# Kernel tuning notes

Measured on AMD Instinct MI355X. Metric: run time of the kernel, lower is better.

## Reference

```python
import jax, jax.numpy as jnp
import numpy as np

N = 50000   # num nodes
E = 800000  # num edges (avg degree 16)
D = 128     # in = hidden = out channels


def setup_inputs() -> dict:
    key = jax.random.key(0)
    k0, k1, k2, k3, k4, k5 = jax.random.split(key, 6)
    x = jax.random.normal(k0, (N, D), dtype=jnp.float32)
    edge_index = jax.random.randint(k1, (2, E), 0, N, dtype=jnp.int32)
    scale = 1.0 / np.sqrt(D)
    W1 = jax.random.normal(k2, (D, D), dtype=jnp.float32) * scale
    b1 = jax.random.normal(k3, (D,), dtype=jnp.float32) * 0.01
    W2 = jax.random.normal(k4, (D, D), dtype=jnp.float32) * scale
    b2 = jax.random.normal(k5, (D,), dtype=jnp.float32) * 0.01
    return {"x": x, "edge_index": edge_index, "W1": W1, "b1": b1, "W2": W2, "b2": b2}


def reference(x, edge_index, W1, b1, W2, b2):
    n = x.shape[0]
    src, dst = edge_index[0], edge_index[1]
    # GCN adds self-loops before normalization
    loops = jnp.arange(n, dtype=src.dtype)
    s = jnp.concatenate([src, loops])
    d = jnp.concatenate([dst, loops])
    # symmetric normalization: deg^{-1/2}[s] * deg^{-1/2}[d]
    deg = jax.ops.segment_sum(jnp.ones_like(d, dtype=x.dtype), d, num_segments=n)
    dinv = jnp.where(deg > 0, jax.lax.rsqrt(deg), 0.0)
    ew = dinv[s] * dinv[d]  # [E+N]

    def gcn_conv(h, W, b):
        h = h @ W                                   # [N, D] dense transform first
        msg = ew[:, None] * h[s]                     # gather over edges [E+N, D]
        agg = jax.ops.segment_sum(msg, d, num_segments=n)  # scatter-add [N, D]
        return agg + b

    # layer 1: conv -> Identity BN -> ELU (dropout=0.0 -> no-op)
    h = jax.nn.elu(gcn_conv(x, W1, b1))
    # layer 2 (last): conv -> Identity BN -> ELU
    out = jax.nn.elu(gcn_conv(h, W2, b2))
    return out
```

## Files before the change

### kernel.cpp

```cpp
#include <hip/hip_runtime.h>
#include <math.h>

#define D 128
#define BCAP 8192
#define SLICE 64
#define PB 256

typedef __attribute__((ext_vector_type(8))) short bf16x8;
typedef __attribute__((ext_vector_type(4))) float f32x4;
typedef __attribute__((ext_vector_type(4))) unsigned int u32x4;


__device__ inline float2 bf2f2(unsigned int u) {
    union { unsigned int i; float f; } a, b;
    a.i = u << 16;
    b.i = u & 0xffff0000u;
    return make_float2(a.f, b.f);
}

__device__ inline unsigned short f2bf(float f) {
    union { float f; unsigned int i; } u;
    u.f = f;
    unsigned int r = u.i + 0x7fffu + ((u.i >> 16) & 1u);
    return (unsigned short)(r >> 16);
}

__device__ __forceinline__ float elu_fast(float r) {
    return r > 0.f ? r : __expf(r) - 1.f;
}


__device__ __forceinline__ void gemm_core(unsigned short (*Ws)[136], int gbid,
                                          const void* __restrict__ Ain, int a_fp32,
                                          unsigned int* __restrict__ Cb, int N) {
    const int tid = threadIdx.x;
    const int wid = tid >> 6;
    const int lane = tid & 63;
    const int quad = lane >> 4;
    const int ln = lane & 15;
    const int m = gbid * 64 + wid * 16 + ln;
    const bool valid = (m < N);

    f32x4 acc[8];
#pragma unroll
    for (int c = 0; c < 8; ++c) acc[c] = (f32x4){0.f, 0.f, 0.f, 0.f};

    __syncthreads();

#pragma unroll
    for (int ks = 0; ks < 4; ++ks) {
        const int k0 = ks * 32;
        bf16x8 af;
        if (a_fp32) {
            const float* A = (const float*)Ain;
            float4 lo = make_float4(0.f, 0.f, 0.f, 0.f), hi = lo;
            if (valid) {
                lo = *(const float4*)&A[(size_t)m * 128 + k0 + quad * 8];
                hi = *(const float4*)&A[(size_t)m * 128 + k0 + quad * 8 + 4];
            }
            af[0] = (short)f2bf(lo.x); af[1] = (short)f2bf(lo.y);
            af[2] = (short)f2bf(lo.z); af[3] = (short)f2bf(lo.w);
            af[4] = (short)f2bf(hi.x); af[5] = (short)f2bf(hi.y);
            af[6] = (short)f2bf(hi.z); af[7] = (short)f2bf(hi.w);
        } else {
            const uint4* A4 = (const uint4*)Ain;
            uint4 v = valid ? A4[(size_t)m * 16 + ks * 4 + quad]
                            : make_uint4(0u, 0u, 0u, 0u);
            union { uint4 u; bf16x8 h; } cv;
            cv.u = v;
            af = cv.h;
        }
#pragma unroll
        for (int c = 0; c < 8; ++c) {
            bf16x8 bf = *(const bf16x8*)&Ws[c * 16 + ln][k0 + quad * 8];
            acc[c] = __builtin_amdgcn_mfma_f32_16x16x32_bf16(af, bf, acc[c], 0, 0, 0);
        }
    }

    const int rowbase = gbid * 64 + wid * 16 + quad * 4;
#pragma unroll
    for (int c = 0; c < 8; ++c) {
#pragma unroll
        for (int r = 0; r < 4; ++r) {
            float v = acc[c][r];
            float vn = __shfl_xor(v, 1);
            int grow = rowbase + r;
            if (!(ln & 1) && grow < N) {
                unsigned int u = (unsigned int)f2bf(v) | ((unsigned int)f2bf(vn) << 16);
                Cb[(size_t)grow * 64 + c * 8 + (ln >> 1)] = u;
            }
        }
    }
}


__global__ __launch_bounds__(256) void k1_all(
        const int* __restrict__ src, const int* __restrict__ dst,
        const float* __restrict__ x, const float* __restrict__ W1,
        const float* __restrict__ W2, unsigned short* __restrict__ Wt2,
        unsigned int* __restrict__ pairs, unsigned char* __restrict__ cellCnt,
        unsigned int* __restrict__ hb1, int e, int chunk, int N, int gemmBlocks) {
    __shared__ __align__(16) unsigned char smem[128 * 136 * 2];
    const int tid = threadIdx.x;
    const int bid = blockIdx.x;

    if (bid < PB) {
        int* cur = (int*)smem;
        cur[tid] = 0;
        __syncthreads();
        const int e0 = bid * chunk;
        const int e1 = min(e0 + chunk, e);
        for (int i = e0 + tid; i < e1; i += 256) {
            int d = dst[i], s = src[i];
            int b = d >> 8;
            int off = atomicAdd(&cur[b], 1);
            if (off < SLICE)
                pairs[((size_t)(bid * 256 + b)) * SLICE + off] =
                    (unsigned int)s | ((unsigned int)(d & 255) << 16);
        }
        __syncthreads();
        cellCnt[bid * 256 + tid] = (unsigned char)min(cur[tid], SLICE);
    } else if (bid < PB + gemmBlocks) {
        unsigned short (*Ws)[136] = (unsigned short(*)[136])smem;
        for (int j = 0; j < 64; ++j) {
            int idx = tid + j * 256;
            Ws[idx & 127][idx >> 7] = f2bf(W1[idx]);
        }
        gemm_core(Ws, bid - PB, x, 1, hb1, N);
    } else {
        int i = (bid - PB - gemmBlocks) * 256 + tid;
        int k = i >> 7, n = i & 127;
        Wt2[n * 128 + k] = f2bf(W2[i]);
    }
}


__global__ __launch_bounds__(1024) void partB(const unsigned int* __restrict__ pairs,
                                              const unsigned char* __restrict__ cellCnt,
                                              unsigned short* __restrict__ col,
                                              unsigned int* __restrict__ meta,
                                              float* __restrict__ dinv, int n) {
    __shared__ unsigned int cellS[256][SLICE];
    __shared__ int cnt[256];
    __shared__ int deg[256];
    __shared__ int sc[256];
    __shared__ int cur[256];
    const int b = blockIdx.x;
    const int tid = threadIdx.x;
    const int cell0 = tid >> 6;
    const int slot = tid & 63;
    const int ch = tid >> 2;
    const int sub = tid & 3;

#pragma unroll
    for (int r = 0; r < 16; ++r) {
        const int cc = r * 16 + cell0;
        cellS[cc][slot] = pairs[((size_t)(cc * 256 + b)) * SLICE + slot];
    }
    if (tid < 256) {
        cnt[tid] = min((int)cellCnt[tid * 256 + b], SLICE);
        deg[tid] = 0;
    }
    __syncthreads();

    const int c = cnt[ch];
    for (int q = sub; q < c; q += 4) atomicAdd(&deg[cellS[ch][q] >> 16], 1);
    __syncthreads();

    if (tid < 256) sc[tid] = deg[tid];
    __syncthreads();
    for (int o = 1; o < 256; o <<= 1) {
        int t = 0;
        if (tid < 256 && tid >= o) t = sc[tid - o];
        __syncthreads();
        if (tid < 256) sc[tid] += t;
        __syncthreads();
    }
    if (tid < 256) {
        int v = deg[tid];
        int startw = sc[tid] - v;
        cur[tid] = startw;
        int node = b * 256 + tid;
        if (node < n) {
            meta[node] = ((unsigned int)(b * BCAP + startw) << 10) | (unsigned int)v;
            dinv[node] = rsqrtf((float)(v + 1));
        }
    }
    __syncthreads();

    for (int q = sub; q < c; q += 4) {
        unsigned int p = cellS[ch][q];
        int dl = p >> 16;
        int off = atomicAdd(&cur[dl], 1);
        col[(size_t)b * BCAP + off] = (unsigned short)(p & 0xffffu);
    }
}


__device__ __forceinline__ void fma8(float w, u32x4 u, f32x4& a, f32x4& b) {
    float2 v0 = bf2f2(u.x), v1 = bf2f2(u.y), v2 = bf2f2(u.z), v3 = bf2f2(u.w);
    a[0] = fmaf(w, v0.x, a[0]); a[1] = fmaf(w, v0.y, a[1]);
    a[2] = fmaf(w, v1.x, a[2]); a[3] = fmaf(w, v1.y, a[3]);
    b[0] = fmaf(w, v2.x, b[0]); b[1] = fmaf(w, v2.y, b[1]);
    b[2] = fmaf(w, v3.x, b[2]); b[3] = fmaf(w, v3.y, b[3]);
}

__device__ __forceinline__ void add8(u32x4 u, f32x4& a, f32x4& b) {
    float2 v0 = bf2f2(u.x), v1 = bf2f2(u.y), v2 = bf2f2(u.z), v3 = bf2f2(u.w);
    a[0] += v0.x; a[1] += v0.y; a[2] += v1.x; a[3] += v1.y;
    b[0] += v2.x; b[1] += v2.y; b[2] += v3.x; b[3] += v3.y;
}

template <bool PRE>
__device__ __forceinline__ float2 agg_wave_rs(const unsigned int* __restrict__ hb,
                                              const unsigned short* __restrict__ col,
                                              const float* __restrict__ dinv,
                                              int node, int g, int ln,
                                              unsigned int m, float di) {
    const u32x4* hb4 = (const u32x4*)hb;
    const int s0 = (int)(m >> 10);
    const int s1 = s0 + (int)(m & 1023u);

    f32x4 sA = (f32x4){0.f, 0.f, 0.f, 0.f};
    f32x4 sB = (f32x4){0.f, 0.f, 0.f, 0.f};
    {
        u32x4 su = hb4[((unsigned)node << 4) + ln];
        float ws = (g == 0) ? (PRE ? 1.f : di) : 0.f;
        fma8(ws, su, sA, sB);
    }

    int i = s0;
    for (; i + 16 <= s1; i += 16) {
        const int c0 = col[i + g];
        const int c1 = col[i + 4 + g];
        const int c2 = col[i + 8 + g];
        const int c3 = col[i + 12 + g];
        float w0 = 0.f, w1 = 0.f, w2 = 0.f, w3 = 0.f;
        if (!PRE) { w0 = dinv[c0]; w1 = dinv[c1]; w2 = dinv[c2]; w3 = dinv[c3]; }
        u32x4 u0 = hb4[((unsigned)c0 << 4) + ln];
        u32x4 u1 = hb4[((unsigned)c1 << 4) + ln];
        u32x4 u2 = hb4[((unsigned)c2 << 4) + ln];
        u32x4 u3 = hb4[((unsigned)c3 << 4) + ln];
        asm volatile("" :: "v"(u0), "v"(u1), "v"(u2), "v"(u3));
        if (PRE) {
            add8(u0, sA, sB); add8(u1, sA, sB);
            add8(u2, sA, sB); add8(u3, sA, sB);
        } else {
            fma8(w0, u0, sA, sB); fma8(w1, u1, sA, sB);
            fma8(w2, u2, sA, sB); fma8(w3, u3, sA, sB);
        }
    }
    while (i < s1) {
        const int t = i + g;
        const bool ok = (t < s1);
        const int cc = ok ? (int)col[t] : node;
        u32x4 u = hb4[((unsigned)cc << 4) + ln];
        if (PRE) {
            if (ok) add8(u, sA, sB);
        } else {
            const float w = ok ? dinv[cc] : 0.f;
            fma8(w, u, sA, sB);
        }
        i += 4;
    }

    f32x4 t;
#pragma unroll
    for (int k = 0; k < 4; ++k) {
        float pa = __shfl_xor(sA[k], 16);
        float pb = __shfl_xor(sB[k], 16);
        t[k] = (g & 1) ? (sB[k] + pb) : (sA[k] + pa);
    }
    float p0 = __shfl_xor(t[0], 32);
    float p1 = __shfl_xor(t[1], 32);
    float p2 = __shfl_xor(t[2], 32);
    float p3 = __shfl_xor(t[3], 32);
    float e0 = (g & 2) ? (t[2] + p2) : (t[0] + p0);
    float e1 = (g & 2) ? (t[3] + p3) : (t[1] + p1);
    return make_float2(e0, e1);
}


__global__ __launch_bounds__(1024, 4) void k3_agg_gemm(
        const unsigned int* __restrict__ hb1, const unsigned int* __restrict__ meta,
        const unsigned short* __restrict__ col, const float* __restrict__ dinv,
        const float* __restrict__ b1, const unsigned short* __restrict__ Wt2,
        unsigned int* __restrict__ hb2, int n) {
    __shared__ unsigned int g1s[16 * 68];
    __shared__ __align__(16) unsigned short Ws[128][136];

    const int tid = threadIdx.x;
    const int wid = tid >> 6;
    const int lane = tid & 63;
    const int g = lane >> 4;
    const int ln = lane & 15;
    const int nodeBase = blockIdx.x * 16;
    const int node = nodeBase + wid;

    {
        const int nloc = tid >> 3;
        const int kb = (tid & 7) * 16;
        const uint4* gp = (const uint4*)(Wt2 + (size_t)nloc * 128 + kb);
        uint4* sp = (uint4*)&Ws[nloc][kb];
        sp[0] = gp[0];
        sp[1] = gp[1];
    }

    const int cp = 4 * ln + 2 * (g & 1) + (g >> 1);
    if (node < n) {
        const unsigned int m = meta[node];
        const float di = dinv[node];
        float2 e = agg_wave_rs<false>(hb1, col, dinv, node, g, ln, m, di);
        const float2 bv = ((const float2*)b1)[cp];
        float r0 = elu_fast(fmaf(di, e.x, bv.x));
        float r1 = elu_fast(fmaf(di, e.y, bv.y));
        g1s[wid * 68 + cp] = (unsigned int)f2bf(r0) | ((unsigned int)f2bf(r1) << 16);
    } else {
        g1s[wid * 68 + cp] = 0u;
    }
    __syncthreads();

    if (wid < 8) {
        const int quad = lane >> 4;
        f32x4 acc = (f32x4){0.f, 0.f, 0.f, 0.f};
#pragma unroll
        for (int ks = 0; ks < 4; ++ks) {
            bf16x8 af = *(const bf16x8*)&g1s[ln * 68 + ks * 16 + quad * 4];
            bf16x8 bf = *(const bf16x8*)&Ws[wid * 16 + ln][ks * 32 + quad * 8];
            acc = __builtin_amdgcn_mfma_f32_16x16x32_bf16(af, bf, acc, 0, 0, 0);
        }
#pragma unroll
        for (int r = 0; r < 4; ++r) {
            int grow = nodeBase + quad * 4 + r;
            float dsc = (grow < n) ? dinv[grow] : 0.f;
            float v = acc[r] * dsc;
            float vn = __shfl_xor(v, 1);
            if (!(ln & 1) && grow < n) {
                hb2[(size_t)grow * 64 + wid * 8 + (ln >> 1)] =
                    (unsigned int)f2bf(v) | ((unsigned int)f2bf(vn) << 16);
            }
        }
    }
}


__global__ __launch_bounds__(256, 4) void agg_elu(const unsigned int* __restrict__ hb,
                                                  const unsigned int* __restrict__ meta,
                                                  const unsigned short* __restrict__ col,
                                                  const float* __restrict__ dinv,
                                                  const float* __restrict__ bias,
                                                  float* __restrict__ outf, int n) {
    const int wid = threadIdx.x >> 6;
    const int lane = threadIdx.x & 63;
    const int g = lane >> 4;
    const int ln = lane & 15;
    const int node = blockIdx.x * 4 + wid;
    if (node >= n) return;

    const unsigned int m = meta[node];
    const float di = dinv[node];
    float2 e = agg_wave_rs<true>(hb, col, dinv, node, g, ln, m, di);

    const int cp = 4 * ln + 2 * (g & 1) + (g >> 1);
    const float2 bv = ((const float2*)bias)[cp];
    float2 r;
    r.x = elu_fast(fmaf(di, e.x, bv.x));
    r.y = elu_fast(fmaf(di, e.y, bv.y));
    ((float2*)outf)[(size_t)node * 64 + cp] = r;
}


extern "C" void kernel_launch(void* const* d_in, const int* in_sizes, int n_in,
                              void* d_out, int out_size, void* d_ws, size_t ws_size,
                              hipStream_t stream) {
    const float* x  = (const float*)d_in[0];
    const int*   ei = (const int*)d_in[1];
    const float* W1 = (const float*)d_in[2];
    const float* b1 = (const float*)d_in[3];
    const float* W2 = (const float*)d_in[4];
    const float* b2 = (const float*)d_in[5];
    float* out = (float*)d_out;

    const int N = in_sizes[0] / D;
    const int E = in_sizes[1] / 2;
    const int* src = ei;
    const int* dst = ei + E;
    const int NB = (N + 255) / 256;

    char* ws = (char*)d_ws;
    size_t off = 0;
    auto alloc = [&](size_t bytes) -> void* {
        void* p = ws + off;
        off = (off + bytes + 255) & ~(size_t)255;
        return p;
    };
    unsigned int*   pairs   = (unsigned int*)alloc((size_t)PB * 256 * SLICE * 4);
    unsigned char*  cellCnt = (unsigned char*)alloc((size_t)PB * 256);
    unsigned short* col     = (unsigned short*)alloc((size_t)NB * BCAP * 2);
    unsigned int*   meta    = (unsigned int*)alloc((size_t)N * 4);
    float*          dinv    = (float*)alloc((size_t)N * 4);
    unsigned short* Wt2     = (unsigned short*)alloc(128 * 128 * 2);
    unsigned int*   hb1     = (unsigned int*)alloc((size_t)N * 64 * 4);
    unsigned int*   hb2     = (unsigned int*)alloc((size_t)N * 64 * 4);
    (void)ws_size; (void)n_in; (void)out_size;

    const int chunk = (E + PB - 1) / PB;
    const int gemmBlocks = (N + 63) / 64;

    k1_all<<<PB + gemmBlocks + 64, 256, 0, stream>>>(src, dst, x, W1, W2, Wt2,
                                                     pairs, cellCnt, hb1, E, chunk,
                                                     N, gemmBlocks);
    partB<<<NB, 1024, 0, stream>>>(pairs, cellCnt, col, meta, dinv, N);
    k3_agg_gemm<<<(N + 15) / 16, 1024, 0, stream>>>(hb1, meta, col, dinv, b1, Wt2, hb2, N);
    agg_elu<<<(N + 3) / 4, 256, 0, stream>>>(hb2, meta, col, dinv, b2, out, N);
}
```

Before: 187.0 us.

## Split partition and GEMM kernels and transpose pairs layout for contiguous bucket reads

Splits the fused first kernel into a separate edge-partition kernel and a GEMM kernel, losing the overlap between them but giving each its own smaller LDS footprint. Transposes the pairs and cellCnt layout so each destination bucket's cells are contiguous, letting partB load them with uint4 vector copies instead of strided scalar loads. Also vectorizes the W1 load into LDS with float4 reads. The partition kernel's scattered writes now go to bucket-major addresses, and the extra launch adds overhead.

```diff
diff --git a/kernel.cpp b/kernel.cpp
--- a/kernel.cpp
+++ b/kernel.cpp
@@ -94,41 +94,53 @@
 }
 
 
-__global__ __launch_bounds__(256) void k1_all(
+__global__ __launch_bounds__(256) void k1_part(
         const int* __restrict__ src, const int* __restrict__ dst,
+        unsigned int* __restrict__ pairs, unsigned char* __restrict__ cellCnt,
+        int e, int chunk) {
+    __shared__ int cur[256];
+    const int tid = threadIdx.x;
+    const int bid = blockIdx.x;
+    cur[tid] = 0;
+    __syncthreads();
+    const int e0 = bid * chunk;
+    const int e1 = min(e0 + chunk, e);
+    for (int i = e0 + tid; i < e1; i += 256) {
+        int d = dst[i], s = src[i];
+        int b = d >> 8;
+        int off = atomicAdd(&cur[b], 1);
+        if (off < SLICE)
+            pairs[((size_t)(b * 256 + bid)) * SLICE + off] =
+                (unsigned int)s | ((unsigned int)(d & 255) << 16);
+    }
+    __syncthreads();
+    cellCnt[(size_t)tid * 256 + bid] = (unsigned char)min(cur[tid], SLICE);
+}
+
+
+__global__ __launch_bounds__(256) void k1_gemm(
         const float* __restrict__ x, const float* __restrict__ W1,
         const float* __restrict__ W2, unsigned short* __restrict__ Wt2,
-        unsigned int* __restrict__ pairs, unsigned char* __restrict__ cellCnt,
-        unsigned int* __restrict__ hb1, int e, int chunk, int N, int gemmBlocks) {
-    __shared__ __align__(16) unsigned char smem[128 * 136 * 2];
+        unsigned int* __restrict__ hb1, int N, int gemmBlocks) {
+    __shared__ __align__(16) unsigned short Ws[128][136];
     const int tid = threadIdx.x;
     const int bid = blockIdx.x;
 
-    if (bid < PB) {
-        int* cur = (int*)smem;
-        cur[tid] = 0;
-        __syncthreads();
-        const int e0 = bid * chunk;
-        const int e1 = min(e0 + chunk, e);
-        for (int i = e0 + tid; i < e1; i += 256) {
-            int d = dst[i], s = src[i];
-            int b = d >> 8;
-            int off = atomicAdd(&cur[b], 1);
-            if (off < SLICE)
-                pairs[((size_t)(bid * 256 + b)) * SLICE + off] =
-                    (unsigned int)s | ((unsigned int)(d & 255) << 16);
-        }
-        __syncthreads();
-        cellCnt[bid * 256 + tid] = (unsigned char)min(cur[tid], SLICE);
-    } else if (bid < PB + gemmBlocks) {
-        unsigned short (*Ws)[136] = (unsigned short(*)[136])smem;
-        for (int j = 0; j < 64; ++j) {
-            int idx = tid + j * 256;
-            Ws[idx & 127][idx >> 7] = f2bf(W1[idx]);
-        }
-        gemm_core(Ws, bid - PB, x, 1, hb1, N);
+    if (bid < gemmBlocks) {
+#pragma unroll
+        for (int j = 0; j < 16; ++j) {
+            const int q = tid + j * 256;
+            const float4 w = ((const float4*)W1)[q];
+            const int k = q >> 5;
+            const int n0 = (q & 31) * 4;
+            Ws[n0 + 0][k] = f2bf(w.x);
+            Ws[n0 + 1][k] = f2bf(w.y);
+            Ws[n0 + 2][k] = f2bf(w.z);
+            Ws[n0 + 3][k] = f2bf(w.w);
+        }
+        gemm_core(Ws, bid, x, 1, hb1, N);
     } else {
-        int i = (bid - PB - gemmBlocks) * 256 + tid;
+        int i = (bid - gemmBlocks) * 256 + tid;
         int k = i >> 7, n = i & 127;
         Wt2[n * 128 + k] = f2bf(W2[i]);
     }
@@ -140,31 +152,30 @@
                                               unsigned short* __restrict__ col,
                                               unsigned int* __restrict__ meta,
                                               float* __restrict__ dinv, int n) {
-    __shared__ unsigned int cellS[256][SLICE];
+    __shared__ unsigned int cellS[256 * SLICE];
     __shared__ int cnt[256];
     __shared__ int deg[256];
     __shared__ int sc[256];
     __shared__ int cur[256];
     const int b = blockIdx.x;
     const int tid = threadIdx.x;
-    const int cell0 = tid >> 6;
-    const int slot = tid & 63;
     const int ch = tid >> 2;
     const int sub = tid & 3;
 
-#pragma unroll
-    for (int r = 0; r < 16; ++r) {
-        const int cc = r * 16 + cell0;
-        cellS[cc][slot] = pairs[((size_t)(cc * 256 + b)) * SLICE + slot];
+    {
+        const uint4* gp = (const uint4*)(pairs + (size_t)b * (256 * SLICE));
+        uint4* sp = (uint4*)cellS;
+#pragma unroll
+        for (int r = 0; r < 4; ++r) sp[tid + r * 1024] = gp[tid + r * 1024];
     }
     if (tid < 256) {
-        cnt[tid] = min((int)cellCnt[tid * 256 + b], SLICE);
+        cnt[tid] = min((int)cellCnt[(size_t)b * 256 + tid], SLICE);
         deg[tid] = 0;
     }
     __syncthreads();
 
     const int c = cnt[ch];
-    for (int q = sub; q < c; q += 4) atomicAdd(&deg[cellS[ch][q] >> 16], 1);
+    for (int q = sub; q < c; q += 4) atomicAdd(&deg[cellS[ch * SLICE + q] >> 16], 1);
     __syncthreads();
 
     if (tid < 256) sc[tid] = deg[tid];
@@ -189,7 +200,7 @@
     __syncthreads();
 
     for (int q = sub; q < c; q += 4) {
-        unsigned int p = cellS[ch][q];
+        unsigned int p = cellS[ch * SLICE + q];
         int dl = p >> 16;
         int off = atomicAdd(&cur[dl], 1);
         col[(size_t)b * BCAP + off] = (unsigned short)(p & 0xffffu);
@@ -394,8 +405,8 @@
         off = (off + bytes + 255) & ~(size_t)255;
         return p;
     };
-    unsigned int*   pairs   = (unsigned int*)alloc((size_t)PB * 256 * SLICE * 4);
-    unsigned char*  cellCnt = (unsigned char*)alloc((size_t)PB * 256);
+    unsigned int*   pairs   = (unsigned int*)alloc((size_t)256 * PB * SLICE * 4);
+    unsigned char*  cellCnt = (unsigned char*)alloc((size_t)256 * PB);
     unsigned short* col     = (unsigned short*)alloc((size_t)NB * BCAP * 2);
     unsigned int*   meta    = (unsigned int*)alloc((size_t)N * 4);
     float*          dinv    = (float*)alloc((size_t)N * 4);
@@ -407,9 +418,8 @@
     const int chunk = (E + PB - 1) / PB;
     const int gemmBlocks = (N + 63) / 64;
 
-    k1_all<<<PB + gemmBlocks + 64, 256, 0, stream>>>(src, dst, x, W1, W2, Wt2,
-                                                     pairs, cellCnt, hb1, E, chunk,
-                                                     N, gemmBlocks);
+    k1_part<<<PB, 256, 0, stream>>>(src, dst, pairs, cellCnt, E, chunk);
+    k1_gemm<<<gemmBlocks + 64, 256, 0, stream>>>(x, W1, W2, Wt2, hb1, N, gemmBlocks);
     partB<<<NB, 1024, 0, stream>>>(pairs, cellCnt, col, meta, dinv, N);
     k3_agg_gemm<<<(N + 15) / 16, 1024, 0, stream>>>(hb1, meta, col, dinv, b1, Wt2, hb2, N);
     agg_elu<<<(N + 3) / 4, 256, 0, stream>>>(hb2, meta, col, dinv, b2, out, N);
```

New measurement: 198.1 us. +5.9%, slower.
